# Optimization experiments

Measured on AMD Instinct MI355X. Metric: run time of the kernel, lower is better.

Reference implementation:

```python
import jax, jax.numpy as jnp
import numpy as np

EMBED_DIM = 1024
NUM_HEADS = 16
HEAD_DIM = EMBED_DIM // NUM_HEADS


def setup_inputs() -> dict:
    key = jax.random.key(0)
    ks = jax.random.split(key, 11)
    B, T, D = 4, 2048, EMBED_DIM
    s = 1.0 / np.sqrt(D)
    inp = {
        "x": jax.random.normal(ks[0], (B, T, D), dtype=jnp.float32),
        "wq": jax.random.normal(ks[1], (D, D), dtype=jnp.float32) * s,
        "bq": jnp.zeros((D,), dtype=jnp.float32),
        "wk": jax.random.normal(ks[2], (D, D), dtype=jnp.float32) * s,
        "bk": jnp.zeros((D,), dtype=jnp.float32),
        "wv": jax.random.normal(ks[3], (D, D), dtype=jnp.float32) * s,
        "bv": jnp.zeros((D,), dtype=jnp.float32),
        "wo": jax.random.normal(ks[4], (D, D), dtype=jnp.float32) * s,
        "bo": jnp.zeros((D,), dtype=jnp.float32),
        "ln_gamma": jnp.ones((D,), dtype=jnp.float32),
        "ln_beta": jnp.zeros((D,), dtype=jnp.float32),
    }
    return inp


def _attention(x, wq, bq, wk, bk, wv, bv, wo, bo, ln_gamma, ln_beta):
    B, T, D = x.shape
    H, Hd = NUM_HEADS, HEAD_DIM
    # projections -> (B, H, T, Hd)
    q = (x @ wq + bq).reshape(B, T, H, Hd).transpose(0, 2, 1, 3)
    k = (x @ wk + bk).reshape(B, T, H, Hd).transpose(0, 2, 1, 3)
    v = (x @ wv + bv).reshape(B, T, H, Hd).transpose(0, 2, 1, 3)
    scores = jnp.einsum("bhqd,bhkd->bhqk", q, k) / jnp.sqrt(jnp.asarray(Hd, x.dtype))
    attn = jax.nn.softmax(scores, axis=-1)  # dropout p=0 -> identity
    out = jnp.einsum("bhqk,bhkd->bhqd", attn, v)
    out = out.transpose(0, 2, 1, 3).reshape(B, T, D)
    out = out @ wo + bo
    # LayerNorm (no residual in the original forward)
    mu = jnp.mean(out, axis=-1, keepdims=True)
    var = jnp.var(out, axis=-1, keepdims=True)
    out = (out - mu) / jnp.sqrt(var + 1e-5) * ln_gamma + ln_beta
    return out


def reference(x, wq, bq, wk, bk, wv, bv, wo, bo, ln_gamma, ln_beta):
    return _attention(x, wq, bq, wk, bk, wv, bv, wo, bo, ln_gamma, ln_beta)
```

## Files before the change

kernel.cpp:

```cpp
#include <hip/hip_runtime.h>
#include <hip/hip_bf16.h>

typedef __bf16 bf16_t;
typedef __bf16 bf16x4v __attribute__((ext_vector_type(4)));
typedef __bf16 bf16x8 __attribute__((ext_vector_type(8)));
typedef float  f32x4  __attribute__((ext_vector_type(4)));

typedef __attribute__((address_space(1))) void* gptr_t;
typedef __attribute__((address_space(3))) void* lptr_t;

#define B_BATCH  4
#define T_SEQ    2048
#define D_MODEL  1024
#define N_HEADS  16
#define HEAD_DIM 64
#define M_ROWS   (B_BATCH * T_SEQ)

#define BM  128
#define BN  128
#define BKK 64
#define PROW 40

#define EXP2_SCALE 0.1803368801111204f

__global__ __launch_bounds__(256) void cvt_x(
    const float* __restrict__ in, bf16_t* __restrict__ out)
{
    const size_t tid = (size_t)blockIdx.x * 256 + threadIdx.x;
    for (int rep = 0; rep < 4; rep++) {
        const size_t i = (tid + (size_t)rep * 524288) * 4;
        const f32x4 v = *(const f32x4*)&in[i];
        bf16x4v o;
        for (int e = 0; e < 4; e++) o[e] = (bf16_t)v[e];
        *(bf16x4v*)&out[i] = o;
    }
}

__global__ __launch_bounds__(256) void transpose_w(
    const float* __restrict__ w0, const float* __restrict__ w1,
    const float* __restrict__ w2, const float* __restrict__ w3,
    bf16_t* __restrict__ out)
{
    __shared__ bf16_t tile[32][33];
    const int z = blockIdx.z;
    const float* w = (z == 0) ? w0 : (z == 1) ? w1 : (z == 2) ? w2 : w3;
    bf16_t* o = out + (size_t)z * D_MODEL * D_MODEL;
    const int tx = threadIdx.x & 31, ty = threadIdx.x >> 5;
    const int k0 = blockIdx.y * 32, n0 = blockIdx.x * 32;
    for (int i = 0; i < 4; i++)
        tile[ty + i * 8][tx] = (bf16_t)w[(size_t)(k0 + ty + i * 8) * D_MODEL + n0 + tx];
    __syncthreads();
    for (int i = 0; i < 4; i++)
        o[(size_t)(n0 + ty + i * 8) * D_MODEL + k0 + tx] = tile[tx][ty + i * 8];
}

__global__ __launch_bounds__(512, 2) void qkv_k(
    const bf16_t* __restrict__ A, const bf16_t* __restrict__ BT,
    const float* __restrict__ bq, const float* __restrict__ bk,
    const float* __restrict__ bv,
    bf16_t* __restrict__ qk_out, bf16_t* __restrict__ vt_out)
{
    __shared__ __attribute__((aligned(16))) bf16_t smem[65536];

    const int tid = threadIdx.x;
    const int f0 = blockIdx.y * 12 + blockIdx.x;
    const int f  = (f0 & 7) * 48 + (f0 >> 3);
    const int n_t = f % 12, m_t = f / 12;
    const int m0 = m_t * 256, n0 = n_t * 256;
    const int z  = n0 >> 10;
    const int w = tid >> 6, lane = tid & 63, quad = lane >> 4, l16 = lane & 15;
    const int wm = w >> 2, wn = w & 3;
    const int srow = lane >> 3;
    const int scol = ((lane & 7) ^ srow) * 8;
    const int rx = l16 & 7;

    f32x4 acc[8][4] = {};

    for (int it = 0; it < 4; it++) {
        const int R = w * 32 + it * 8;
        __builtin_amdgcn_global_load_lds(
            (gptr_t)&A [(size_t)(m0 + R + srow) * D_MODEL + scol],
            (lptr_t)&smem[R * 64], 16, 0, 0);
        __builtin_amdgcn_global_load_lds(
            (gptr_t)&BT[(size_t)(n0 + R + srow) * D_MODEL + scol],
            (lptr_t)&smem[32768 + R * 64], 16, 0, 0);
    }

    for (int t = 0; t < 16; t++) {
        __syncthreads();
        const bf16_t* Ac = &smem[(t & 1) * 16384];
        const bf16_t* Bc = &smem[32768 + (t & 1) * 16384];
        bf16_t* An = &smem[((t + 1) & 1) * 16384];
        bf16_t* Bn = &smem[32768 + ((t + 1) & 1) * 16384];
        const int kb = (t + 1) * 64;
        const bool pf = (t + 1 < 16);

        #pragma unroll
        for (int s = 0; s < 2; s++) {
            const int rc = ((quad + s * 4) ^ rx) * 8;
            bf16x8 bfr[4];
            #pragma unroll
            for (int j = 0; j < 4; j++)
                bfr[j] = *(const bf16x8*)&Bc[(wn * 64 + j * 16 + l16) * 64 + rc];
            #pragma unroll
            for (int ih = 0; ih < 2; ih++) {
                if (pf) {
                    const int it = s * 2 + ih;
                    const int R = w * 32 + it * 8;
                    __builtin_amdgcn_global_load_lds(
                        (gptr_t)&A [(size_t)(m0 + R + srow) * D_MODEL + kb + scol],
                        (lptr_t)&An[R * 64], 16, 0, 0);
                    __builtin_amdgcn_global_load_lds(
                        (gptr_t)&BT[(size_t)(n0 + R + srow) * D_MODEL + kb + scol],
                        (lptr_t)&Bn[R * 64], 16, 0, 0);
                }
                bf16x8 af[4];
                #pragma unroll
                for (int i = 0; i < 4; i++)
                    af[i] = *(const bf16x8*)
                        &Ac[(wm * 128 + (ih * 4 + i) * 16 + l16) * 64 + rc];
                __builtin_amdgcn_s_setprio(1);
                #pragma unroll
                for (int i = 0; i < 4; i++)
                    #pragma unroll
                    for (int j = 0; j < 4; j++)
                        acc[ih * 4 + i][j] = __builtin_amdgcn_mfma_f32_16x16x32_bf16(
                            af[i], bfr[j], acc[ih * 4 + i][j], 0, 0, 0);
                __builtin_amdgcn_s_setprio(0);
            }
        }
    }

    __syncthreads();

    const float* bias = (z == 0) ? bq : (z == 1) ? bk : bv;
    const int ncol0 = n0 & 1023;
    float bj[4];
    for (int j = 0; j < 4; j++)
        bj[j] = bias[ncol0 + wn * 64 + j * 16 + l16];

    bf16_t (*Cs)[256] = reinterpret_cast<bf16_t(*)[256]>(smem);
    if (z < 2) {
        for (int ai = 0; ai < 8; ai++)
            for (int r = 0; r < 4; r++) {
                const int row = wm * 128 + ai * 16 + quad * 4 + r;
                for (int j = 0; j < 4; j++)
                    Cs[row][wn * 64 + j * 16 + l16] = (bf16_t)(acc[ai][j][r] + bj[j]);
            }
    } else {
        for (int ai = 0; ai < 8; ai++)
            for (int r = 0; r < 4; r++) {
                const int row = wm * 128 + ai * 16 + quad * 4 + r;
                for (int j = 0; j < 4; j++)
                    Cs[wn * 64 + j * 16 + l16][row] = (bf16_t)(acc[ai][j][r] + bj[j]);
            }
    }
    __syncthreads();

    const int bidx = m0 >> 11, t0 = m0 & 2047, hbase = ncol0 >> 6;
    if (z < 2) {
        bf16_t* outp = qk_out + (size_t)z * ((size_t)M_ROWS * D_MODEL);
        for (int p = 0; p < 16; p++) {
            const int chunk = p * 512 + tid;
            const int sub = chunk & 7, hl = (chunk >> 3) & 3, tt = chunk >> 5;
            const bf16x8 val = *(const bf16x8*)&Cs[tt][hl * 64 + sub * 8];
            *(bf16x8*)&outp[(((size_t)(bidx * N_HEADS + hbase + hl)) * T_SEQ + t0 + tt)
                            * HEAD_DIM + sub * 8] = val;
        }
    } else {
        for (int p = 0; p < 16; p++) {
            const int chunk = p * 512 + tid;
            const int sub = chunk & 31, r = chunk >> 5;
            const int h = hbase + (r >> 6), hd = r & 63;
            const bf16x8 val = *(const bf16x8*)&Cs[r][sub * 8];
            *(bf16x8*)&vt_out[(((size_t)(bidx * N_HEADS + h)) * HEAD_DIM + hd) * T_SEQ
                              + t0 + sub * 8] = val;
        }
    }
}

__global__ __launch_bounds__(256) void proj_k(
    const bf16_t* __restrict__ A, const bf16_t* __restrict__ BT,
    const float* __restrict__ bias, float* __restrict__ out)
{
    __shared__ __attribute__((aligned(16))) bf16_t smem[16384];
    bf16_t (*As)[BKK] = reinterpret_cast<bf16_t(*)[BKK]>(&smem[0]);
    bf16_t (*Bs)[BKK] = reinterpret_cast<bf16_t(*)[BKK]>(&smem[8192]);

    const int tid  = threadIdx.x;
    const int mbase = blockIdx.y * BM;
    const int nbase = blockIdx.x * BN;
    const int w = tid >> 6, lane = tid & 63, quad = lane >> 4, l16 = lane & 15;
    const int wm = (w & 1) * 64, wn = (w >> 1) * 64;
    const int lrow = lane >> 3, lcol = (lane & 7) * 8;

    f32x4 acc[4][4] = {};

    for (int kb = 0; kb < D_MODEL; kb += BKK) {
        __syncthreads();
        for (int it = 0; it < 4; it++) {
            const int r = w * 32 + it * 8;
            __builtin_amdgcn_global_load_lds(
                (gptr_t)&A [(size_t)(mbase + r + lrow) * D_MODEL + kb + lcol],
                (lptr_t)&As[r][0], 16, 0, 0);
            __builtin_amdgcn_global_load_lds(
                (gptr_t)&BT[(size_t)(nbase + r + lrow) * D_MODEL + kb + lcol],
                (lptr_t)&Bs[r][0], 16, 0, 0);
        }
        __syncthreads();
        for (int s = 0; s < 2; s++) {
            bf16x8 af[4], bfr[4];
            for (int i = 0; i < 4; i++)
                af[i] = *(const bf16x8*)&As[wm + i * 16 + l16][s * 32 + quad * 8];
            for (int j = 0; j < 4; j++)
                bfr[j] = *(const bf16x8*)&Bs[wn + j * 16 + l16][s * 32 + quad * 8];
            for (int i = 0; i < 4; i++)
                for (int j = 0; j < 4; j++)
                    acc[i][j] = __builtin_amdgcn_mfma_f32_16x16x32_bf16(
                        af[i], bfr[j], acc[i][j], 0, 0, 0);
        }
    }

    float bj[4];
    for (int j = 0; j < 4; j++)
        bj[j] = bias[nbase + wn + j * 16 + l16];

    for (int i = 0; i < 4; i++)
        for (int r = 0; r < 4; r++) {
            const int rg = mbase + wm + i * 16 + quad * 4 + r;
            for (int j = 0; j < 4; j++) {
                const int cg = nbase + wn + j * 16 + l16;
                out[(size_t)rg * D_MODEL + cg] = acc[i][j][r] + bj[j];
            }
        }
}

__global__ __launch_bounds__(256, 4) void attn_k(
    const bf16_t* __restrict__ Q, const bf16_t* __restrict__ K,
    const bf16_t* __restrict__ VT, bf16_t* __restrict__ O)
{
    __shared__ __attribute__((aligned(16))) bf16_t Ks[2][64 * 64];
    __shared__ __attribute__((aligned(16))) bf16_t Vs[64 * 64];
    __shared__ __attribute__((aligned(16))) bf16_t Ps[4][32][PROW];

    const int tid = threadIdx.x;
    const int f = blockIdx.y * 16 + blockIdx.x;
    const int xcd = f & 7, j = f >> 3;
    const int bh = xcd * 8 + (j & 7);
    const int qbase = (j >> 3) * 128;
    const int b = bh >> 4, h = bh & 15;
    const int w = tid >> 6, lane = tid & 63, quad = lane >> 4, l16 = lane & 15;
    const size_t head_off = (size_t)bh * T_SEQ * HEAD_DIM;
    const bf16_t* Qh  = Q  + head_off;
    const bf16_t* Kh  = K  + head_off;
    const bf16_t* VTh = VT + head_off;

    const int srow = lane >> 3;
    const int scol = ((lane & 7) ^ srow) * 8;

    const int rxor = l16 & 7;
    const int rc0 = ((0 + quad) ^ rxor) * 8;
    const int rc1 = ((4 + quad) ^ rxor) * 8;

    bf16x8 bq[2][2];
    for (int iq = 0; iq < 2; iq++)
        for (int s = 0; s < 2; s++)
            bq[iq][s] = *(const bf16x8*)
                &Qh[(size_t)(qbase + w * 32 + iq * 16 + l16) * HEAD_DIM + s * 32 + quad * 8];

    for (int it = 0; it < 2; it++) {
        const int R = w * 16 + it * 8;
        __builtin_amdgcn_global_load_lds(
            (gptr_t)&Kh[(size_t)(R + srow) * HEAD_DIM + scol],
            (lptr_t)&Ks[0][R * 64], 16, 0, 0);
    }

    float l_part[2] = {0.f, 0.f};
    f32x4 Oacc[2][4] = {};

    for (int kt = 0; kt < T_SEQ / 64; kt++) {
        const int kbase = kt * 64;
        __syncthreads();
        const bf16_t* Kc = Ks[kt & 1];

        for (int it = 0; it < 2; it++) {
            const int R = w * 16 + it * 8;
            __builtin_amdgcn_global_load_lds(
                (gptr_t)&VTh[(size_t)(R + srow) * T_SEQ + kbase + scol],
                (lptr_t)&Vs[R * 64], 16, 0, 0);
        }
        if (kt + 1 < T_SEQ / 64) {
            bf16_t* Kn = Ks[(kt + 1) & 1];
            for (int it = 0; it < 2; it++) {
                const int R = w * 16 + it * 8;
                __builtin_amdgcn_global_load_lds(
                    (gptr_t)&Kh[(size_t)(kbase + 64 + R + srow) * HEAD_DIM + scol],
                    (lptr_t)&Kn[R * 64], 16, 0, 0);
            }
        }

        f32x4 St[4][2] = {};
        for (int s = 0; s < 2; s++) {
            const int rc = s ? rc1 : rc0;
            bf16x8 ak[4];
            for (int jk = 0; jk < 4; jk++)
                ak[jk] = *(const bf16x8*)&Kc[(jk * 16 + l16) * 64 + rc];
            __builtin_amdgcn_s_setprio(1);
            for (int jk = 0; jk < 4; jk++)
                for (int iq = 0; iq < 2; iq++)
                    St[jk][iq] = __builtin_amdgcn_mfma_f32_16x16x32_bf16(
                        ak[jk], bq[iq][s], St[jk][iq], 0, 0, 0);
            __builtin_amdgcn_s_setprio(0);
        }

        for (int kk = 0; kk < 2; kk++)
            for (int iq = 0; iq < 2; iq++) {
                bf16x4v pv;
                for (int r = 0; r < 4; r++) {
                    const float p = __builtin_amdgcn_exp2f(St[kk][iq][r] * EXP2_SCALE);
                    l_part[iq] += p;
                    pv[r] = (bf16_t)p;
                }
                *(bf16x4v*)&Ps[w][iq * 16 + l16][kk * 16 + quad * 4] = pv;
            }
        asm volatile("" ::: "memory");

        __syncthreads();

        {
            bf16x8 ap[2], bv4[4];
            for (int iq = 0; iq < 2; iq++)
                ap[iq] = *(const bf16x8*)&Ps[w][iq * 16 + l16][quad * 8];
            for (int jn = 0; jn < 4; jn++)
                bv4[jn] = *(const bf16x8*)&Vs[(jn * 16 + l16) * 64 + rc0];
            __builtin_amdgcn_s_setprio(1);
            for (int iq = 0; iq < 2; iq++)
                for (int jn = 0; jn < 4; jn++)
                    Oacc[iq][jn] = __builtin_amdgcn_mfma_f32_16x16x32_bf16(
                        ap[iq], bv4[jn], Oacc[iq][jn], 0, 0, 0);
            __builtin_amdgcn_s_setprio(0);
        }

        for (int kk = 0; kk < 2; kk++)
            for (int iq = 0; iq < 2; iq++) {
                bf16x4v pv;
                for (int r = 0; r < 4; r++) {
                    const float p = __builtin_amdgcn_exp2f(St[2 + kk][iq][r] * EXP2_SCALE);
                    l_part[iq] += p;
                    pv[r] = (bf16_t)p;
                }
                *(bf16x4v*)&Ps[w][iq * 16 + l16][kk * 16 + quad * 4] = pv;
            }
        asm volatile("" ::: "memory");

        {
            bf16x8 ap[2], bv4[4];
            for (int iq = 0; iq < 2; iq++)
                ap[iq] = *(const bf16x8*)&Ps[w][iq * 16 + l16][quad * 8];
            for (int jn = 0; jn < 4; jn++)
                bv4[jn] = *(const bf16x8*)&Vs[(jn * 16 + l16) * 64 + rc1];
            __builtin_amdgcn_s_setprio(1);
            for (int iq = 0; iq < 2; iq++)
                for (int jn = 0; jn < 4; jn++)
                    Oacc[iq][jn] = __builtin_amdgcn_mfma_f32_16x16x32_bf16(
                        ap[iq], bv4[jn], Oacc[iq][jn], 0, 0, 0);
            __builtin_amdgcn_s_setprio(0);
        }
    }

    for (int iq = 0; iq < 2; iq++) {
        l_part[iq] += __shfl_xor(l_part[iq], 16, 64);
        l_part[iq] += __shfl_xor(l_part[iq], 32, 64);
    }

    for (int iq = 0; iq < 2; iq++) {
        for (int r = 0; r < 4; r++) {
            const int qrow = quad * 4 + r;
            const float inv = 1.f / __shfl(l_part[iq], qrow, 64);
            const int t = qbase + w * 32 + iq * 16 + qrow;
            for (int jn = 0; jn < 4; jn++) {
                const int hd = jn * 16 + l16;
                O[(((size_t)(b * T_SEQ + t)) * N_HEADS + h) * HEAD_DIM + hd] =
                    (bf16_t)(Oacc[iq][jn][r] * inv);
            }
        }
    }
}

__global__ __launch_bounds__(256) void ln_k(
    const float* __restrict__ proj, const float* __restrict__ gamma,
    const float* __restrict__ beta, float* __restrict__ out)
{
    const int tid = threadIdx.x;
    const int w = tid >> 6, lane = tid & 63;
    const int row = blockIdx.x * 4 + w;
    const float* p = proj + (size_t)row * D_MODEL;
    f32x4 v[4];
    float s1 = 0.f, s2 = 0.f;
    for (int e = 0; e < 4; e++) {
        v[e] = *(const f32x4*)&p[e * 256 + lane * 4];
        for (int k = 0; k < 4; k++) { s1 += v[e][k]; s2 += v[e][k] * v[e][k]; }
    }
    for (int off = 32; off >= 1; off >>= 1) {
        s1 += __shfl_xor(s1, off, 64);
        s2 += __shfl_xor(s2, off, 64);
    }
    const float mu  = s1 * (1.f / D_MODEL);
    const float var = s2 * (1.f / D_MODEL) - mu * mu;
    const float rstd = rsqrtf(var + 1e-5f);
    float* o = out + (size_t)row * D_MODEL;
    for (int e = 0; e < 4; e++) {
        const int c = e * 256 + lane * 4;
        const f32x4 g4 = *(const f32x4*)&gamma[c];
        const f32x4 b4 = *(const f32x4*)&beta[c];
        f32x4 ov;
        for (int k = 0; k < 4; k++) ov[k] = (v[e][k] - mu) * rstd * g4[k] + b4[k];
        *(f32x4*)&o[c] = ov;
    }
}

extern "C" void kernel_launch(void* const* d_in, const int* in_sizes, int n_in,
                              void* d_out, int out_size, void* d_ws, size_t ws_size,
                              hipStream_t stream)
{
    const float* x  = (const float*)d_in[0];
    const float* wq = (const float*)d_in[1];
    const float* bq = (const float*)d_in[2];
    const float* wk = (const float*)d_in[3];
    const float* bk = (const float*)d_in[4];
    const float* wv = (const float*)d_in[5];
    const float* bv = (const float*)d_in[6];
    const float* wo = (const float*)d_in[7];
    const float* bo = (const float*)d_in[8];
    const float* g  = (const float*)d_in[9];
    const float* be = (const float*)d_in[10];

    char* ws = (char*)d_ws;
    bf16_t* xb   = (bf16_t*)(ws);
    bf16_t* wT   = (bf16_t*)(ws + ((size_t)16 << 20));
    bf16_t* qkv  = (bf16_t*)(ws + ((size_t)24 << 20));
    bf16_t* attn = (bf16_t*)(ws + ((size_t)72 << 20));
    float*  proj = (float*) (ws + ((size_t)88 << 20));
    bf16_t* vt   = (bf16_t*)proj;

    cvt_x<<<dim3(2048), 256, 0, stream>>>(x, xb);
    transpose_w<<<dim3(32, 32, 4), 256, 0, stream>>>(wq, wk, wv, wo, wT);

    qkv_k<<<dim3(12, 32), 512, 0, stream>>>(xb, wT, bq, bk, bv, qkv, vt);

    bf16_t* Qm = qkv;
    bf16_t* Km = qkv + (size_t)M_ROWS * D_MODEL;

    attn_k<<<dim3(16, 64), 256, 0, stream>>>(Qm, Km, vt, attn);

    proj_k<<<dim3(8, 64), 256, 0, stream>>>(
        attn, wT + (size_t)3 * D_MODEL * D_MODEL, bo, (float*)proj);

    ln_k<<<dim3(M_ROWS / 4), 256, 0, stream>>>(proj, g, be, (float*)d_out);
}
```

Before: 296.4 us.

## Retile QKV GEMM, pipeline output projection, fold softmax scale, MFMA row sums

The QKV GEMM moves to 256x128 tiles with a larger grid and reduced LDS. The output projection is replaced with the double-buffered, XOR-swizzled 256x128 pipeline used for QKV. The exp2 softmax scale is folded into Q at projection time, and the attention row-sum is accumulated with an extra MFMA against a ones vector instead of VALU adds and shuffles. The row sum now accumulates bf16-rounded probabilities, and Q is stored pre-scaled in bf16, which slightly changes numerics.

```diff
diff --git a/kernel.cpp b/kernel.cpp
--- a/kernel.cpp
+++ b/kernel.cpp
@@ -16,9 +16,6 @@
 #define HEAD_DIM 64
 #define M_ROWS   (B_BATCH * T_SEQ)
 
-#define BM  128
-#define BN  128
-#define BKK 64
 #define PROW 40
 
 #define EXP2_SCALE 0.1803368801111204f
@@ -60,27 +57,30 @@
     const float* __restrict__ bv,
     bf16_t* __restrict__ qk_out, bf16_t* __restrict__ vt_out)
 {
-    __shared__ __attribute__((aligned(16))) bf16_t smem[65536];
+    __shared__ __attribute__((aligned(16))) bf16_t smem[49152];
 
     const int tid = threadIdx.x;
-    const int f0 = blockIdx.y * 12 + blockIdx.x;
-    const int f  = (f0 & 7) * 48 + (f0 >> 3);
-    const int n_t = f % 12, m_t = f / 12;
-    const int m0 = m_t * 256, n0 = n_t * 256;
+    const int f0 = blockIdx.y * 24 + blockIdx.x;
+    const int f  = (f0 & 7) * 96 + (f0 >> 3);
+    const int n_t = f % 24, m_t = f / 24;
+    const int m0 = m_t * 256, n0 = n_t * 128;
     const int z  = n0 >> 10;
     const int w = tid >> 6, lane = tid & 63, quad = lane >> 4, l16 = lane & 15;
-    const int wm = w >> 2, wn = w & 3;
+    const int wm = w >> 1, wn = w & 1;
     const int srow = lane >> 3;
     const int scol = ((lane & 7) ^ srow) * 8;
     const int rx = l16 & 7;
 
-    f32x4 acc[8][4] = {};
+    f32x4 acc[4][4] = {};
 
     for (int it = 0; it < 4; it++) {
         const int R = w * 32 + it * 8;
         __builtin_amdgcn_global_load_lds(
-            (gptr_t)&A [(size_t)(m0 + R + srow) * D_MODEL + scol],
+            (gptr_t)&A[(size_t)(m0 + R + srow) * D_MODEL + scol],
             (lptr_t)&smem[R * 64], 16, 0, 0);
+    }
+    for (int it = 0; it < 2; it++) {
+        const int R = w * 16 + it * 8;
         __builtin_amdgcn_global_load_lds(
             (gptr_t)&BT[(size_t)(n0 + R + srow) * D_MODEL + scol],
             (lptr_t)&smem[32768 + R * 64], 16, 0, 0);
@@ -89,9 +89,9 @@
     for (int t = 0; t < 16; t++) {
         __syncthreads();
         const bf16_t* Ac = &smem[(t & 1) * 16384];
-        const bf16_t* Bc = &smem[32768 + (t & 1) * 16384];
+        const bf16_t* Bc = &smem[32768 + (t & 1) * 8192];
         bf16_t* An = &smem[((t + 1) & 1) * 16384];
-        bf16_t* Bn = &smem[32768 + ((t + 1) & 1) * 16384];
+        bf16_t* Bn = &smem[32768 + ((t + 1) & 1) * 8192];
         const int kb = (t + 1) * 64;
         const bool pf = (t + 1 < 16);
 
@@ -102,134 +102,170 @@
             #pragma unroll
             for (int j = 0; j < 4; j++)
                 bfr[j] = *(const bf16x8*)&Bc[(wn * 64 + j * 16 + l16) * 64 + rc];
-            #pragma unroll
-            for (int ih = 0; ih < 2; ih++) {
-                if (pf) {
-                    const int it = s * 2 + ih;
-                    const int R = w * 32 + it * 8;
-                    __builtin_amdgcn_global_load_lds(
-                        (gptr_t)&A [(size_t)(m0 + R + srow) * D_MODEL + kb + scol],
-                        (lptr_t)&An[R * 64], 16, 0, 0);
-                    __builtin_amdgcn_global_load_lds(
-                        (gptr_t)&BT[(size_t)(n0 + R + srow) * D_MODEL + kb + scol],
-                        (lptr_t)&Bn[R * 64], 16, 0, 0);
-                }
-                bf16x8 af[4];
+            if (pf) {
+                const int RA0 = w * 32 + (s * 2) * 8;
+                __builtin_amdgcn_global_load_lds(
+                    (gptr_t)&A[(size_t)(m0 + RA0 + srow) * D_MODEL + kb + scol],
+                    (lptr_t)&An[RA0 * 64], 16, 0, 0);
+                const int RA1 = w * 32 + (s * 2 + 1) * 8;
+                __builtin_amdgcn_global_load_lds(
+                    (gptr_t)&A[(size_t)(m0 + RA1 + srow) * D_MODEL + kb + scol],
+                    (lptr_t)&An[RA1 * 64], 16, 0, 0);
+                const int RB = w * 16 + s * 8;
+                __builtin_amdgcn_global_load_lds(
+                    (gptr_t)&BT[(size_t)(n0 + RB + srow) * D_MODEL + kb + scol],
+                    (lptr_t)&Bn[RB * 64], 16, 0, 0);
+            }
+            bf16x8 af[4];
+            #pragma unroll
+            for (int i = 0; i < 4; i++)
+                af[i] = *(const bf16x8*)&Ac[(wm * 64 + i * 16 + l16) * 64 + rc];
+            __builtin_amdgcn_s_setprio(1);
+            #pragma unroll
+            for (int i = 0; i < 4; i++)
                 #pragma unroll
-                for (int i = 0; i < 4; i++)
-                    af[i] = *(const bf16x8*)
-                        &Ac[(wm * 128 + (ih * 4 + i) * 16 + l16) * 64 + rc];
-                __builtin_amdgcn_s_setprio(1);
-                #pragma unroll
-                for (int i = 0; i < 4; i++)
-                    #pragma unroll
-                    for (int j = 0; j < 4; j++)
-                        acc[ih * 4 + i][j] = __builtin_amdgcn_mfma_f32_16x16x32_bf16(
-                            af[i], bfr[j], acc[ih * 4 + i][j], 0, 0, 0);
-                __builtin_amdgcn_s_setprio(0);
-            }
+                for (int j = 0; j < 4; j++)
+                    acc[i][j] = __builtin_amdgcn_mfma_f32_16x16x32_bf16(
+                        af[i], bfr[j], acc[i][j], 0, 0, 0);
+            __builtin_amdgcn_s_setprio(0);
         }
     }
 
     __syncthreads();
 
     const float* bias = (z == 0) ? bq : (z == 1) ? bk : bv;
+    const float qscale = (z == 0) ? EXP2_SCALE : 1.0f;
     const int ncol0 = n0 & 1023;
     float bj[4];
     for (int j = 0; j < 4; j++)
         bj[j] = bias[ncol0 + wn * 64 + j * 16 + l16];
 
-    bf16_t (*Cs)[256] = reinterpret_cast<bf16_t(*)[256]>(smem);
-    if (z < 2) {
-        for (int ai = 0; ai < 8; ai++)
-            for (int r = 0; r < 4; r++) {
-                const int row = wm * 128 + ai * 16 + quad * 4 + r;
-                for (int j = 0; j < 4; j++)
-                    Cs[row][wn * 64 + j * 16 + l16] = (bf16_t)(acc[ai][j][r] + bj[j]);
-            }
-    } else {
-        for (int ai = 0; ai < 8; ai++)
-            for (int r = 0; r < 4; r++) {
-                const int row = wm * 128 + ai * 16 + quad * 4 + r;
-                for (int j = 0; j < 4; j++)
-                    Cs[wn * 64 + j * 16 + l16][row] = (bf16_t)(acc[ai][j][r] + bj[j]);
-            }
-    }
-    __syncthreads();
-
     const int bidx = m0 >> 11, t0 = m0 & 2047, hbase = ncol0 >> 6;
     if (z < 2) {
+        bf16_t (*Cs)[136] = reinterpret_cast<bf16_t(*)[136]>(smem);
+        for (int ai = 0; ai < 4; ai++)
+            for (int r = 0; r < 4; r++) {
+                const int row = wm * 64 + ai * 16 + quad * 4 + r;
+                for (int j = 0; j < 4; j++)
+                    Cs[row][wn * 64 + j * 16 + l16] =
+                        (bf16_t)((acc[ai][j][r] + bj[j]) * qscale);
+            }
+        __syncthreads();
         bf16_t* outp = qk_out + (size_t)z * ((size_t)M_ROWS * D_MODEL);
-        for (int p = 0; p < 16; p++) {
+        for (int p = 0; p < 8; p++) {
             const int chunk = p * 512 + tid;
-            const int sub = chunk & 7, hl = (chunk >> 3) & 3, tt = chunk >> 5;
-            const bf16x8 val = *(const bf16x8*)&Cs[tt][hl * 64 + sub * 8];
+            const int sub = chunk & 15, tt = chunk >> 4;
+            const int hl = sub >> 3, sub8 = sub & 7;
+            const bf16x8 val = *(const bf16x8*)&Cs[tt][hl * 64 + sub8 * 8];
             *(bf16x8*)&outp[(((size_t)(bidx * N_HEADS + hbase + hl)) * T_SEQ + t0 + tt)
-                            * HEAD_DIM + sub * 8] = val;
+                            * HEAD_DIM + sub8 * 8] = val;
         }
     } else {
-        for (int p = 0; p < 16; p++) {
+        bf16_t (*CsV)[264] = reinterpret_cast<bf16_t(*)[264]>(smem);
+        for (int ai = 0; ai < 4; ai++)
+            for (int r = 0; r < 4; r++) {
+                const int row = wm * 64 + ai * 16 + quad * 4 + r;
+                for (int j = 0; j < 4; j++)
+                    CsV[wn * 64 + j * 16 + l16][row] = (bf16_t)(acc[ai][j][r] + bj[j]);
+            }
+        __syncthreads();
+        for (int p = 0; p < 8; p++) {
             const int chunk = p * 512 + tid;
             const int sub = chunk & 31, r = chunk >> 5;
             const int h = hbase + (r >> 6), hd = r & 63;
-            const bf16x8 val = *(const bf16x8*)&Cs[r][sub * 8];
+            const bf16x8 val = *(const bf16x8*)&CsV[r][sub * 8];
             *(bf16x8*)&vt_out[(((size_t)(bidx * N_HEADS + h)) * HEAD_DIM + hd) * T_SEQ
                               + t0 + sub * 8] = val;
         }
     }
 }
 
-__global__ __launch_bounds__(256) void proj_k(
+__global__ __launch_bounds__(512, 2) void proj_k(
     const bf16_t* __restrict__ A, const bf16_t* __restrict__ BT,
     const float* __restrict__ bias, float* __restrict__ out)
 {
-    __shared__ __attribute__((aligned(16))) bf16_t smem[16384];
-    bf16_t (*As)[BKK] = reinterpret_cast<bf16_t(*)[BKK]>(&smem[0]);
-    bf16_t (*Bs)[BKK] = reinterpret_cast<bf16_t(*)[BKK]>(&smem[8192]);
-
-    const int tid  = threadIdx.x;
-    const int mbase = blockIdx.y * BM;
-    const int nbase = blockIdx.x * BN;
+    __shared__ __attribute__((aligned(16))) bf16_t smem[49152];
+
+    const int tid = threadIdx.x;
+    const int f0 = blockIdx.y * 8 + blockIdx.x;
+    const int f  = (f0 & 7) * 32 + (f0 >> 3);
+    const int n_t = f & 7, m_t = f >> 3;
+    const int m0 = m_t * 256, n0 = n_t * 128;
     const int w = tid >> 6, lane = tid & 63, quad = lane >> 4, l16 = lane & 15;
-    const int wm = (w & 1) * 64, wn = (w >> 1) * 64;
-    const int lrow = lane >> 3, lcol = (lane & 7) * 8;
+    const int wm = w >> 1, wn = w & 1;
+    const int srow = lane >> 3;
+    const int scol = ((lane & 7) ^ srow) * 8;
+    const int rx = l16 & 7;
 
     f32x4 acc[4][4] = {};
 
-    for (int kb = 0; kb < D_MODEL; kb += BKK) {
-        __syncthreads();
-        for (int it = 0; it < 4; it++) {
-            const int r = w * 32 + it * 8;
-            __builtin_amdgcn_global_load_lds(
-                (gptr_t)&A [(size_t)(mbase + r + lrow) * D_MODEL + kb + lcol],
-                (lptr_t)&As[r][0], 16, 0, 0);
-            __builtin_amdgcn_global_load_lds(
-                (gptr_t)&BT[(size_t)(nbase + r + lrow) * D_MODEL + kb + lcol],
-                (lptr_t)&Bs[r][0], 16, 0, 0);
-        }
-        __syncthreads();
+    for (int it = 0; it < 4; it++) {
+        const int R = w * 32 + it * 8;
+        __builtin_amdgcn_global_load_lds(
+            (gptr_t)&A[(size_t)(m0 + R + srow) * D_MODEL + scol],
+            (lptr_t)&smem[R * 64], 16, 0, 0);
+    }
+    for (int it = 0; it < 2; it++) {
+        const int R = w * 16 + it * 8;
+        __builtin_amdgcn_global_load_lds(
+            (gptr_t)&BT[(size_t)(n0 + R + srow) * D_MODEL + scol],
+            (lptr_t)&smem[32768 + R * 64], 16, 0, 0);
+    }
+
+    for (int t = 0; t < 16; t++) {
+        __syncthreads();
+        const bf16_t* Ac = &smem[(t & 1) * 16384];
+        const bf16_t* Bc = &smem[32768 + (t & 1) * 8192];
+        bf16_t* An = &smem[((t + 1) & 1) * 16384];
+        bf16_t* Bn = &smem[32768 + ((t + 1) & 1) * 8192];
+        const int kb = (t + 1) * 64;
+        const bool pf = (t + 1 < 16);
+
+        #pragma unroll
         for (int s = 0; s < 2; s++) {
-            bf16x8 af[4], bfr[4];
+            const int rc = ((quad + s * 4) ^ rx) * 8;
+            bf16x8 bfr[4];
+            #pragma unroll
+            for (int j = 0; j < 4; j++)
+                bfr[j] = *(const bf16x8*)&Bc[(wn * 64 + j * 16 + l16) * 64 + rc];
+            if (pf) {
+                const int RA0 = w * 32 + (s * 2) * 8;
+                __builtin_amdgcn_global_load_lds(
+                    (gptr_t)&A[(size_t)(m0 + RA0 + srow) * D_MODEL + kb + scol],
+                    (lptr_t)&An[RA0 * 64], 16, 0, 0);
+                const int RA1 = w * 32 + (s * 2 + 1) * 8;
+                __builtin_amdgcn_global_load_lds(
+                    (gptr_t)&A[(size_t)(m0 + RA1 + srow) * D_MODEL + kb + scol],
+                    (lptr_t)&An[RA1 * 64], 16, 0, 0);
+                const int RB = w * 16 + s * 8;
+                __builtin_amdgcn_global_load_lds(
+                    (gptr_t)&BT[(size_t)(n0 + RB + srow) * D_MODEL + kb + scol],
+                    (lptr_t)&Bn[RB * 64], 16, 0, 0);
+            }
+            bf16x8 af[4];
+            #pragma unroll
             for (int i = 0; i < 4; i++)
-                af[i] = *(const bf16x8*)&As[wm + i * 16 + l16][s * 32 + quad * 8];
-            for (int j = 0; j < 4; j++)
-                bfr[j] = *(const bf16x8*)&Bs[wn + j * 16 + l16][s * 32 + quad * 8];
+                af[i] = *(const bf16x8*)&Ac[(wm * 64 + i * 16 + l16) * 64 + rc];
+            __builtin_amdgcn_s_setprio(1);
+            #pragma unroll
             for (int i = 0; i < 4; i++)
+                #pragma unroll
                 for (int j = 0; j < 4; j++)
                     acc[i][j] = __builtin_amdgcn_mfma_f32_16x16x32_bf16(
                         af[i], bfr[j], acc[i][j], 0, 0, 0);
+            __builtin_amdgcn_s_setprio(0);
         }
     }
 
     float bj[4];
     for (int j = 0; j < 4; j++)
-        bj[j] = bias[nbase + wn + j * 16 + l16];
+        bj[j] = bias[n0 + wn * 64 + j * 16 + l16];
 
     for (int i = 0; i < 4; i++)
         for (int r = 0; r < 4; r++) {
-            const int rg = mbase + wm + i * 16 + quad * 4 + r;
+            const int rg = m0 + wm * 64 + i * 16 + quad * 4 + r;
             for (int j = 0; j < 4; j++) {
-                const int cg = nbase + wn + j * 16 + l16;
+                const int cg = n0 + wn * 64 + j * 16 + l16;
                 out[(size_t)rg * D_MODEL + cg] = acc[i][j][r] + bj[j];
             }
         }
@@ -268,6 +304,9 @@
             bq[iq][s] = *(const bf16x8*)
                 &Qh[(size_t)(qbase + w * 32 + iq * 16 + l16) * HEAD_DIM + s * 32 + quad * 8];
 
+    bf16x8 vone;
+    for (int e = 0; e < 8; e++) vone[e] = (bf16_t)1.0f;
+
     for (int it = 0; it < 2; it++) {
         const int R = w * 16 + it * 8;
         __builtin_amdgcn_global_load_lds(
@@ -275,8 +314,8 @@
             (lptr_t)&Ks[0][R * 64], 16, 0, 0);
     }
 
-    float l_part[2] = {0.f, 0.f};
     f32x4 Oacc[2][4] = {};
+    f32x4 lacc[2] = {};
 
     for (int kt = 0; kt < T_SEQ / 64; kt++) {
         const int kbase = kt * 64;
@@ -316,11 +355,8 @@
         for (int kk = 0; kk < 2; kk++)
             for (int iq = 0; iq < 2; iq++) {
                 bf16x4v pv;
-                for (int r = 0; r < 4; r++) {
-                    const float p = __builtin_amdgcn_exp2f(St[kk][iq][r] * EXP2_SCALE);
-                    l_part[iq] += p;
-                    pv[r] = (bf16_t)p;
-                }
+                for (int r = 0; r < 4; r++)
+                    pv[r] = (bf16_t)__builtin_amdgcn_exp2f(St[kk][iq][r]);
                 *(bf16x4v*)&Ps[w][iq * 16 + l16][kk * 16 + quad * 4] = pv;
             }
         asm volatile("" ::: "memory");
@@ -334,21 +370,21 @@
             for (int jn = 0; jn < 4; jn++)
                 bv4[jn] = *(const bf16x8*)&Vs[(jn * 16 + l16) * 64 + rc0];
             __builtin_amdgcn_s_setprio(1);
-            for (int iq = 0; iq < 2; iq++)
+            for (int iq = 0; iq < 2; iq++) {
                 for (int jn = 0; jn < 4; jn++)
                     Oacc[iq][jn] = __builtin_amdgcn_mfma_f32_16x16x32_bf16(
                         ap[iq], bv4[jn], Oacc[iq][jn], 0, 0, 0);
+                lacc[iq] = __builtin_amdgcn_mfma_f32_16x16x32_bf16(
+                    ap[iq], vone, lacc[iq], 0, 0, 0);
+            }
             __builtin_amdgcn_s_setprio(0);
         }
 
         for (int kk = 0; kk < 2; kk++)
             for (int iq = 0; iq < 2; iq++) {
                 bf16x4v pv;
-                for (int r = 0; r < 4; r++) {
-                    const float p = __builtin_amdgcn_exp2f(St[2 + kk][iq][r] * EXP2_SCALE);
-                    l_part[iq] += p;
-                    pv[r] = (bf16_t)p;
-                }
+                for (int r = 0; r < 4; r++)
+                    pv[r] = (bf16_t)__builtin_amdgcn_exp2f(St[2 + kk][iq][r]);
                 *(bf16x4v*)&Ps[w][iq * 16 + l16][kk * 16 + quad * 4] = pv;
             }
         asm volatile("" ::: "memory");
@@ -360,24 +396,21 @@
             for (int jn = 0; jn < 4; jn++)
                 bv4[jn] = *(const bf16x8*)&Vs[(jn * 16 + l16) * 64 + rc1];
             __builtin_amdgcn_s_setprio(1);
-            for (int iq = 0; iq < 2; iq++)
+            for (int iq = 0; iq < 2; iq++) {
                 for (int jn = 0; jn < 4; jn++)
                     Oacc[iq][jn] = __builtin_amdgcn_mfma_f32_16x16x32_bf16(
                         ap[iq], bv4[jn], Oacc[iq][jn], 0, 0, 0);
+                lacc[iq] = __builtin_amdgcn_mfma_f32_16x16x32_bf16(
+                    ap[iq], vone, lacc[iq], 0, 0, 0);
+            }
             __builtin_amdgcn_s_setprio(0);
         }
-    }
-
-    for (int iq = 0; iq < 2; iq++) {
-        l_part[iq] += __shfl_xor(l_part[iq], 16, 64);
-        l_part[iq] += __shfl_xor(l_part[iq], 32, 64);
     }
 
     for (int iq = 0; iq < 2; iq++) {
         for (int r = 0; r < 4; r++) {
-            const int qrow = quad * 4 + r;
-            const float inv = 1.f / __shfl(l_part[iq], qrow, 64);
-            const int t = qbase + w * 32 + iq * 16 + qrow;
+            const float inv = 1.f / lacc[iq][r];
+            const int t = qbase + w * 32 + iq * 16 + quad * 4 + r;
             for (int jn = 0; jn < 4; jn++) {
                 const int hd = jn * 16 + l16;
                 O[(((size_t)(b * T_SEQ + t)) * N_HEADS + h) * HEAD_DIM + hd] =
@@ -446,14 +479,14 @@
     cvt_x<<<dim3(2048), 256, 0, stream>>>(x, xb);
     transpose_w<<<dim3(32, 32, 4), 256, 0, stream>>>(wq, wk, wv, wo, wT);
 
-    qkv_k<<<dim3(12, 32), 512, 0, stream>>>(xb, wT, bq, bk, bv, qkv, vt);
+    qkv_k<<<dim3(24, 32), 512, 0, stream>>>(xb, wT, bq, bk, bv, qkv, vt);
 
     bf16_t* Qm = qkv;
     bf16_t* Km = qkv + (size_t)M_ROWS * D_MODEL;
 
     attn_k<<<dim3(16, 64), 256, 0, stream>>>(Qm, Km, vt, attn);
 
-    proj_k<<<dim3(8, 64), 256, 0, stream>>>(
+    proj_k<<<dim3(8, 32), 512, 0, stream>>>(
         attn, wT + (size_t)3 * D_MODEL * D_MODEL, bo, (float*)proj);
 
     ln_k<<<dim3(M_ROWS / 4), 256, 0, stream>>>(proj, g, be, (float*)d_out);
```

Result: faster. 274.6 us (-7.3%).
